# Kernel tuning notes

Measured on AMD Instinct MI355X. Metric: run time of the kernel, lower is better.

Reference implementation:

```python
import jax, jax.numpy as jnp
import numpy as np

SD = 4          # spixel_downsize
EPS = 1e-5      # BatchNorm eps
SLOPE = 0.01    # nn.LeakyReLU() default negative_slope


def deconv3d(x, w, stride, pad):
    # w is in torch ConvTranspose3d layout: (in_ch, out_ch, kd, kh, kw).
    # Transposed conv == conv with lhs_dilation=stride, flipped kernel,
    # padding (k-1-p) per spatial dim.
    kd, kh, kw = w.shape[2], w.shape[3], w.shape[4]
    wc = jnp.transpose(jnp.flip(w, axis=(2, 3, 4)), (1, 0, 2, 3, 4))  # OIDHW
    pads = [(kd - 1 - pad[0],) * 2, (kh - 1 - pad[1],) * 2, (kw - 1 - pad[2],) * 2]
    return jax.lax.conv_general_dilated(
        x, wc, window_strides=(1, 1, 1), padding=pads,
        lhs_dilation=(stride, stride, stride),
        dimension_numbers=('NCDHW', 'OIDHW', 'NCDHW'))


def bn_lrelu(x, g, b, relu=True):
    # inference BatchNorm3d with running_mean=0, running_var=1 (fresh BN)
    scale = (g / jnp.sqrt(1.0 + EPS)).reshape(1, -1, 1, 1, 1)
    y = x * scale + b.reshape(1, -1, 1, 1, 1)
    return jax.nn.leaky_relu(y, SLOPE) if relu else y


def _sl(s):
    # shift s in {+1, 0, -1} -> (agg slice, cost slice) along one spatial dim
    if s == 1:
        return slice(SD, None), slice(None, -SD)
    if s == 0:
        return slice(None), slice(None)
    return slice(None, -SD), slice(SD, None)


def setup_inputs() -> dict:
    key = jax.random.key(0)
    ks = jax.random.split(key, 8)
    b, d, h, w = 1, 24, 64, 128
    f32 = jnp.float32
    cv1 = jax.random.normal(ks[0], (b, 32, d, h, w), f32)                 # cv[-1]
    cv0 = jax.random.normal(ks[1], (b, 16, 2 * d, 2 * h, 2 * w), f32)     # cv[-2]
    sp = jax.random.uniform(ks[2], (b, 9, 4 * h, 4 * w), f32)             # superpixel probs
    w0a = jax.random.normal(ks[3], (32, 32, 3, 1, 1), f32) * 0.05
    w0b = jax.random.normal(ks[4], (32, 16, 4, 2, 2), f32) * 0.05
    w1a = jax.random.normal(ks[5], (32, 16, 3, 1, 1), f32) * 0.05
    w1b = jax.random.normal(ks[6], (16, 1, 4, 2, 2), f32) * 0.05
    g0, g1, g2, g3 = (jnp.ones((c,), f32) for c in (32, 16, 16, 1))
    b0, b1, b2, b3 = (jnp.zeros((c,), f32) for c in (32, 16, 16, 1))
    return dict(cv1=cv1, cv0=cv0, sp=sp, w0a=w0a, w0b=w0b, w1a=w1a, w1b=w1b,
                g0=g0, g1=g1, g2=g2, g3=g3, b0=b0, b1=b1, b2=b2, b3=b3)


def reference(cv1, cv0, sp, w0a, w0b, w1a, w1b, g0, g1, g2, g3, b0, b1, b2, b3):
    # conv[0]: BasicConv(32->32, k(3,1,1), s1, p(1,0,0)) + BasicConv(32->16, k(4,2,2), s2, p(1,0,0))
    x = bn_lrelu(deconv3d(cv1, w0a, 1, (1, 0, 0)), g0, b0)
    x = bn_lrelu(deconv3d(x, w0b, 2, (1, 0, 0)), g1, b1)
    x = jnp.concatenate((x, cv0), axis=1)
    # conv[1] (sp==2 branch): 32->16 then 16->out_dim, bn=relu=bnrelu=True
    x = bn_lrelu(deconv3d(x, w1a, 1, (1, 0, 0)), g2, b2)
    cost = bn_lrelu(deconv3d(x, w1b, 2, (1, 0, 0)), g3, b3)  # (b, 1, 4d, 4h, 4w)

    sp5 = sp[:, None]  # (b, 1, 9, H, W)
    agg = jnp.zeros_like(cost)
    k = 0
    for hy in (1, 0, -1):        # 9 fixed superpixel-neighbor shifts
        ah, ch = _sl(hy)
        for wx in (1, 0, -1):
            aw, cw = _sl(wx)
            wgt = sp5[:, :, k, ah, aw][:, :, None]  # (b,1,1,H',W')
            agg = agg.at[:, :, :, ah, aw].add(cost[:, :, :, ch, cw] * wgt)
            k += 1
    return agg
```

## Files before the change

kernel.cpp:

```cpp
#include <hip/hip_runtime.h>
#include <hip/hip_bf16.h>

typedef __hip_bfloat16 bf16;

constexpr int cD0 = 24,  cH0 = 64,  cW0 = 128;
constexpr int cD1 = 48,  cH1 = 128, cW1 = 256;
constexpr int cD2 = 96,  cH2 = 256, cW2 = 512;
constexpr size_t PL0 = (size_t)cD0 * cH0 * cW0;
constexpr size_t PL1 = (size_t)cD1 * cH1 * cW1;
constexpr size_t PL2 = (size_t)cD2 * cH2 * cW2;

__device__ __forceinline__ float b2f(bf16 v) { return __bfloat162float(v); }
__device__ __forceinline__ bf16  f2b(float v) { return __float2bfloat16(v); }
__device__ __forceinline__ float lrelu(float v) { return v >= 0.f ? v : 0.01f * v; }
__device__ __forceinline__ float us2f(ushort u) { return __uint_as_float(((uint)u) << 16); }
__device__ __forceinline__ ushort f2us(float v) { return __bfloat16_as_ushort(f2b(v)); }

__global__ __launch_bounds__(256) void kA(const float* __restrict__ cv1,
                                          const float* __restrict__ w0a,
                                          const float* __restrict__ g0,
                                          const float* __restrict__ b0,
                                          bf16* __restrict__ x1) {
    __shared__ float lw[3][32][32];
    __shared__ float lsc[32], lbi[32];
    const int tid = threadIdx.x;
    for (int i = tid; i < 32 * 32 * 3; i += 256) {
        int ci = i / 96, r = i - ci * 96, co = r / 3, u = r - co * 3;
        lw[u][ci][co] = w0a[i];
    }
    if (tid < 32) {
        lsc[tid] = g0[tid] * (1.0f / sqrtf(1.0f + 1e-5f));
        lbi[tid] = b0[tid];
    }
    __syncthreads();

    const int pos = blockIdx.x * 256 + tid;
    const int x = pos & (cW0 - 1);
    const int y = (pos >> 7) & (cH0 - 1);
    const int z = pos >> 13;

    float acc[32];
    #pragma unroll
    for (int co = 0; co < 32; ++co) acc[co] = 0.f;

    #pragma unroll
    for (int u = 0; u < 3; ++u) {
        const int zi = z + 1 - u;
        if (zi < 0 || zi >= cD0) continue;
        const float* src = cv1 + (size_t)(zi * cH0 + y) * cW0 + x;
        for (int ci = 0; ci < 32; ++ci) {
            const float v = src[ci * PL0];
            const float4* wp = (const float4*)&lw[u][ci][0];
            #pragma unroll
            for (int q = 0; q < 8; ++q) {
                float4 wv = wp[q];
                acc[4*q+0] += v * wv.x; acc[4*q+1] += v * wv.y;
                acc[4*q+2] += v * wv.z; acc[4*q+3] += v * wv.w;
            }
        }
    }
    #pragma unroll
    for (int co = 0; co < 32; ++co)
        x1[co * PL0 + (size_t)(z * cH0 + y) * cW0 + x] =
            f2b(lrelu(acc[co] * lsc[co] + lbi[co]));
}

__global__ __launch_bounds__(256) void kB(const bf16* __restrict__ x1,
                                          const float* __restrict__ w0b,
                                          const float* __restrict__ g1,
                                          const float* __restrict__ b1,
                                          bf16* __restrict__ x2) {
    __shared__ float lw[4][2][32][2][16];
    __shared__ float lsc[16], lbi[16];
    const int tid = threadIdx.x;
    for (int i = tid; i < 8192; i += 256) {
        int ci = i >> 8, co = (i >> 4) & 15, kd = (i >> 2) & 3, kh = (i >> 1) & 1, kw = i & 1;
        lw[kd][kh][ci][kw][co] = w0b[i];
    }
    if (tid < 16) {
        lsc[tid] = g1[tid] * (1.0f / sqrtf(1.0f + 1e-5f));
        lbi[tid] = b1[tid];
    }
    __syncthreads();

    const int t    = blockIdx.x * 256 + tid;
    const int lane = t & 63;
    const int row  = t >> 6;
    const int oh = row & 127, od = row >> 7;
    const int ih = oh >> 1, kh = oh & 1;
    const int p  = (od + 1) & 1;
    const int iw0 = 2 * lane;

    float acc[4][16];
    #pragma unroll
    for (int k = 0; k < 4; ++k)
        #pragma unroll
        for (int co = 0; co < 16; ++co) acc[k][co] = 0.f;

    #pragma unroll
    for (int j = 0; j < 2; ++j) {
        const int kd = p + 2 * j;
        const int id = (od + 1 - kd) >> 1;
        if (id < 0 || id >= cD0) continue;
        const bf16* src = x1 + (size_t)(id * cH0 + ih) * cW0 + iw0;
        #pragma unroll 4
        for (int ci = 0; ci < 32; ++ci) {
            const uint pk = *(const uint*)(src + ci * PL0);
            const float v0 = us2f((ushort)(pk & 0xffffu));
            const float v1 = us2f((ushort)(pk >> 16));
            const float4* wp0 = (const float4*)&lw[kd][kh][ci][0][0];
            const float4* wp1 = (const float4*)&lw[kd][kh][ci][1][0];
            #pragma unroll
            for (int q = 0; q < 4; ++q) {
                float4 w0 = wp0[q], w1 = wp1[q];
                acc[0][4*q+0] += v0 * w0.x; acc[0][4*q+1] += v0 * w0.y;
                acc[0][4*q+2] += v0 * w0.z; acc[0][4*q+3] += v0 * w0.w;
                acc[1][4*q+0] += v0 * w1.x; acc[1][4*q+1] += v0 * w1.y;
                acc[1][4*q+2] += v0 * w1.z; acc[1][4*q+3] += v0 * w1.w;
                acc[2][4*q+0] += v1 * w0.x; acc[2][4*q+1] += v1 * w0.y;
                acc[2][4*q+2] += v1 * w0.z; acc[2][4*q+3] += v1 * w0.w;
                acc[3][4*q+0] += v1 * w1.x; acc[3][4*q+1] += v1 * w1.y;
                acc[3][4*q+2] += v1 * w1.z; acc[3][4*q+3] += v1 * w1.w;
            }
        }
    }
    const size_t obase = (size_t)(od * cH1 + oh) * cW1 + 4 * lane;
    #pragma unroll
    for (int co = 0; co < 16; ++co) {
        ushort4 s;
        s.x = f2us(lrelu(acc[0][co] * lsc[co] + lbi[co]));
        s.y = f2us(lrelu(acc[1][co] * lsc[co] + lbi[co]));
        s.z = f2us(lrelu(acc[2][co] * lsc[co] + lbi[co]));
        s.w = f2us(lrelu(acc[3][co] * lsc[co] + lbi[co]));
        *(ushort4*)(x2 + co * PL1 + obase) = s;
    }
}

__global__ __launch_bounds__(256) void kD(const bf16* __restrict__ x2,
                                          const float* __restrict__ cv0,
                                          const float* __restrict__ w1a,
                                          const float* __restrict__ g2,
                                          const float* __restrict__ b2v,
                                          bf16* __restrict__ x3) {
    __shared__ float lw[3][32][16];
    __shared__ float lsc[16], lbi[16];
    const int tid = threadIdx.x;
    for (int i = tid; i < 1536; i += 256) {
        int ci = i / 48, r = i - ci * 48, co = r / 3, u = r - co * 3;
        lw[u][ci][co] = w1a[i];
    }
    if (tid < 16) {
        lsc[tid] = g2[tid] * (1.0f / sqrtf(1.0f + 1e-5f));
        lbi[tid] = b2v[tid];
    }
    __syncthreads();

    const int t    = blockIdx.x * 256 + tid;
    const int lane = t & 63;
    const int row  = t >> 6;
    const int y = row & 127, z = row >> 7;
    const int x0 = 4 * lane;

    float acc[4][16];
    #pragma unroll
    for (int k = 0; k < 4; ++k)
        #pragma unroll
        for (int co = 0; co < 16; ++co) acc[k][co] = 0.f;

    #pragma unroll
    for (int u = 0; u < 3; ++u) {
        const int zi = z + 1 - u;
        if (zi < 0 || zi >= cD1) continue;
        const size_t base = (size_t)(zi * cH1 + y) * cW1 + x0;
        #pragma unroll 4
        for (int ci = 0; ci < 16; ++ci) {
            const ushort4 pv = *(const ushort4*)(x2 + ci * PL1 + base);
            const float v0 = us2f(pv.x), v1 = us2f(pv.y);
            const float v2 = us2f(pv.z), v3 = us2f(pv.w);
            const float4* wp = (const float4*)&lw[u][ci][0];
            #pragma unroll
            for (int q = 0; q < 4; ++q) {
                float4 wv = wp[q];
                acc[0][4*q+0] += v0 * wv.x; acc[0][4*q+1] += v0 * wv.y;
                acc[0][4*q+2] += v0 * wv.z; acc[0][4*q+3] += v0 * wv.w;
                acc[1][4*q+0] += v1 * wv.x; acc[1][4*q+1] += v1 * wv.y;
                acc[1][4*q+2] += v1 * wv.z; acc[1][4*q+3] += v1 * wv.w;
                acc[2][4*q+0] += v2 * wv.x; acc[2][4*q+1] += v2 * wv.y;
                acc[2][4*q+2] += v2 * wv.z; acc[2][4*q+3] += v2 * wv.w;
                acc[3][4*q+0] += v3 * wv.x; acc[3][4*q+1] += v3 * wv.y;
                acc[3][4*q+2] += v3 * wv.z; acc[3][4*q+3] += v3 * wv.w;
            }
        }
        #pragma unroll 4
        for (int ci = 0; ci < 16; ++ci) {
            const float4 fv = *(const float4*)(cv0 + ci * PL1 + base);
            const float v0 = fv.x, v1 = fv.y, v2 = fv.z, v3 = fv.w;
            const float4* wp = (const float4*)&lw[u][16 + ci][0];
            #pragma unroll
            for (int q = 0; q < 4; ++q) {
                float4 wv = wp[q];
                acc[0][4*q+0] += v0 * wv.x; acc[0][4*q+1] += v0 * wv.y;
                acc[0][4*q+2] += v0 * wv.z; acc[0][4*q+3] += v0 * wv.w;
                acc[1][4*q+0] += v1 * wv.x; acc[1][4*q+1] += v1 * wv.y;
                acc[1][4*q+2] += v1 * wv.z; acc[1][4*q+3] += v1 * wv.w;
                acc[2][4*q+0] += v2 * wv.x; acc[2][4*q+1] += v2 * wv.y;
                acc[2][4*q+2] += v2 * wv.z; acc[2][4*q+3] += v2 * wv.w;
                acc[3][4*q+0] += v3 * wv.x; acc[3][4*q+1] += v3 * wv.y;
                acc[3][4*q+2] += v3 * wv.z; acc[3][4*q+3] += v3 * wv.w;
            }
        }
    }
    const size_t obase = (size_t)(z * cH1 + y) * cW1 + x0;
    #pragma unroll
    for (int co = 0; co < 16; ++co) {
        ushort4 s;
        s.x = f2us(lrelu(acc[0][co] * lsc[co] + lbi[co]));
        s.y = f2us(lrelu(acc[1][co] * lsc[co] + lbi[co]));
        s.z = f2us(lrelu(acc[2][co] * lsc[co] + lbi[co]));
        s.w = f2us(lrelu(acc[3][co] * lsc[co] + lbi[co]));
        *(ushort4*)(x3 + co * PL1 + obase) = s;
    }
}

__global__ __launch_bounds__(256) void kE(const bf16* __restrict__ x3,
                                          const float* __restrict__ w1b,
                                          const float* __restrict__ g3,
                                          const float* __restrict__ b3v,
                                          bf16* __restrict__ cost) {
    __shared__ float lw[256];
    const int tid = threadIdx.x;
    lw[tid] = w1b[tid];
    __syncthreads();

    const int t    = blockIdx.x * 256 + tid;
    const int lane = t & 63;
    const int rowq = t >> 6;
    const int iwp = lane + 64 * (rowq & 1);
    const int ih  = (rowq >> 1) & 127;
    const int od  = rowq >> 8;
    const int p   = (od + 1) & 1;
    const int iw0 = 2 * iwp;

    float a[2][2][2] = {};
    #pragma unroll
    for (int j = 0; j < 2; ++j) {
        const int kd = p + 2 * j;
        const int id = (od + 1 - kd) >> 1;
        if (id < 0 || id >= cD1) continue;
        const size_t base = (size_t)(id * cH1 + ih) * cW1 + iw0;
        #pragma unroll
        for (int ci = 0; ci < 16; ++ci) {
            const uint pk = *(const uint*)(x3 + ci * PL1 + base);
            const float v0 = us2f((ushort)(pk & 0xffffu));
            const float v1 = us2f((ushort)(pk >> 16));
            const float* w = &lw[ci * 16 + kd * 4];
            a[0][0][0] += v0 * w[0]; a[0][0][1] += v0 * w[1];
            a[0][1][0] += v0 * w[2]; a[0][1][1] += v0 * w[3];
            a[1][0][0] += v1 * w[0]; a[1][0][1] += v1 * w[1];
            a[1][1][0] += v1 * w[2]; a[1][1][1] += v1 * w[3];
        }
    }
    const float sc = g3[0] * (1.0f / sqrtf(1.0f + 1e-5f));
    const float bi = b3v[0];
    const size_t ob = (size_t)(od * cH2 + 2 * ih) * cW2 + 4 * iwp;
    ushort4 s;
    s.x = f2us(lrelu(a[0][0][0] * sc + bi));
    s.y = f2us(lrelu(a[0][0][1] * sc + bi));
    s.z = f2us(lrelu(a[1][0][0] * sc + bi));
    s.w = f2us(lrelu(a[1][0][1] * sc + bi));
    *(ushort4*)(cost + ob) = s;
    s.x = f2us(lrelu(a[0][1][0] * sc + bi));
    s.y = f2us(lrelu(a[0][1][1] * sc + bi));
    s.z = f2us(lrelu(a[1][1][0] * sc + bi));
    s.w = f2us(lrelu(a[1][1][1] * sc + bi));
    *(ushort4*)(cost + ob + cW2) = s;
}

__global__ __launch_bounds__(256) void kF(const bf16* __restrict__ cost,
                                          const float* __restrict__ sp,
                                          float* __restrict__ out) {
    const int t    = blockIdx.x * 256 + threadIdx.x;
    const int lane = t & 63;
    const int rowq = t >> 6;
    const int x0 = 4 * (lane + 64 * (rowq & 1));
    const int y  = (rowq >> 1) & 255;
    const int d0 = (rowq >> 9) * 4;
    const size_t plane = (size_t)cH2 * cW2;

    float4 wq[9];
    int cyc[3], cxc[3];
    #pragma unroll
    for (int r = 0; r < 3; ++r) {
        const int cy = y - 4 * (1 - r);
        const bool vy = (cy >= 0) && (cy < cH2);
        cyc[r] = vy ? cy : 0;
        #pragma unroll
        for (int c = 0; c < 3; ++c) {
            const int cx = x0 - 4 * (1 - c);
            const bool vx = (cx >= 0) && (cx < cW2);
            if (r == 0) cxc[c] = vx ? cx : 0;
            if (vy && vx)
                wq[r*3+c] = *(const float4*)(sp + (size_t)(r*3+c) * plane + (size_t)y * cW2 + x0);
            else
                wq[r*3+c] = make_float4(0.f, 0.f, 0.f, 0.f);
        }
    }
    #pragma unroll
    for (int dd = 0; dd < 4; ++dd) {
        const int d = d0 + dd;
        const bf16* cp = cost + (size_t)d * plane;
        float ax = 0.f, ay = 0.f, az = 0.f, aw = 0.f;
        #pragma unroll
        for (int r = 0; r < 3; ++r) {
            const bf16* rp = cp + (size_t)cyc[r] * cW2;
            #pragma unroll
            for (int c = 0; c < 3; ++c) {
                const ushort4 u = *(const ushort4*)(rp + cxc[c]);
                const float4 w = wq[r*3+c];
                ax += w.x * us2f(u.x); ay += w.y * us2f(u.y);
                az += w.z * us2f(u.z); aw += w.w * us2f(u.w);
            }
        }
        float4 o; o.x = ax; o.y = ay; o.z = az; o.w = aw;
        *(float4*)(out + (size_t)d * plane + (size_t)y * cW2 + x0) = o;
    }
}

extern "C" void kernel_launch(void* const* d_in, const int* in_sizes, int n_in,
                              void* d_out, int out_size, void* d_ws, size_t ws_size,
                              hipStream_t stream) {
    const float* cv1 = (const float*)d_in[0];
    const float* cv0 = (const float*)d_in[1];
    const float* sp  = (const float*)d_in[2];
    const float* w0a = (const float*)d_in[3];
    const float* w0b = (const float*)d_in[4];
    const float* w1a = (const float*)d_in[5];
    const float* w1b = (const float*)d_in[6];
    const float* g0  = (const float*)d_in[7];
    const float* g1  = (const float*)d_in[8];
    const float* g2  = (const float*)d_in[9];
    const float* g3  = (const float*)d_in[10];
    const float* b0  = (const float*)d_in[11];
    const float* b1  = (const float*)d_in[12];
    const float* b2  = (const float*)d_in[13];
    const float* b3  = (const float*)d_in[14];

    char* ws = (char*)d_ws;
    bf16* x1   = (bf16*)(ws);
    bf16* x2   = (bf16*)(ws + 12582912);
    bf16* x3   = (bf16*)(ws + 62914560);
    bf16* cost = (bf16*)(ws);

    kA<<<768,  256, 0, stream>>>(cv1, w0a, g0, b0, x1);
    kB<<<1536, 256, 0, stream>>>(x1, w0b, g1, b1, x2);
    kD<<<1536, 256, 0, stream>>>(x2, cv0, w1a, g2, b2, x3);
    kE<<<6144, 256, 0, stream>>>(x3, w1b, g3, b3, cost);
    kF<<<3072, 256, 0, stream>>>(cost, sp, (float*)d_out);
}
```

Baseline: 402.9 us.

## Remap wave-to-row assignment and interleave kw across lanes in deconv kernels

Kernels kC, kD and kE now give the four waves of a block four consecutive depth slices at the same (h) row instead of four consecutive h rows. Waves in a block therefore share overlapping input planes along depth, which may improve cache reuse. In kC each lane now handles a single kw parity and four input columns spaced 32 apart, so its bf16 stores are per-element and coalesced rather than ushort4. The trade-offs are scalar 2-byte loads and stores in place of packed accesses, and half the weights per lane in the inner loop.

Measured after the change: 383.5 us. 4.8% less time.

```diff
diff --git a/kernel.cpp b/kernel.cpp
--- a/kernel.cpp
+++ b/kernel.cpp
@@ -85,11 +85,14 @@
 
     const int t    = blockIdx.x * 256 + tid;
     const int lane = t & 63;
-    const int row  = t >> 6;
-    const int oh = row & 127, od = row >> 7;
+    const int wv_  = (t >> 6) & 3;
+    const int b_   = t >> 8;
+    const int oh = b_ & 127;
+    const int od = (b_ >> 7) * 4 + wv_;
     const int ih = oh >> 1, kh = oh & 1;
+    const int kw = lane & 1;
     const int p  = (od + 1) & 1;
-    const int iw0 = 2 * lane;
+    const int iwb = lane >> 1;
 
     float acc[4][16];
     #pragma unroll
@@ -102,38 +105,34 @@
         const int kd = p + 2 * j;
         const int id = (od + 1 - kd) >> 1;
         if (id < 0 || id >= cD0) continue;
-        const bf16* src = x1 + (size_t)(id * cH0 + ih) * cW0 + iw0;
-        #pragma unroll 4
+        const bf16* src = x1 + (size_t)(id * cH0 + ih) * cW0 + iwb;
         for (int ci = 0; ci < 32; ++ci) {
-            const uint pk = *(const uint*)(src + ci * PL0);
-            const float v0 = us2f((ushort)(pk & 0xffffu));
-            const float v1 = us2f((ushort)(pk >> 16));
-            const float4* wp0 = (const float4*)&lw[kd][kh][ci][0][0];
-            const float4* wp1 = (const float4*)&lw[kd][kh][ci][1][0];
+            const float v0 = b2f(src[ci * PL0 +  0]);
+            const float v1 = b2f(src[ci * PL0 + 32]);
+            const float v2 = b2f(src[ci * PL0 + 64]);
+            const float v3 = b2f(src[ci * PL0 + 96]);
+            const float4* wp = (const float4*)&lw[kd][kh][ci][kw][0];
             #pragma unroll
             for (int q = 0; q < 4; ++q) {
-                float4 w0 = wp0[q], w1 = wp1[q];
-                acc[0][4*q+0] += v0 * w0.x; acc[0][4*q+1] += v0 * w0.y;
-                acc[0][4*q+2] += v0 * w0.z; acc[0][4*q+3] += v0 * w0.w;
-                acc[1][4*q+0] += v0 * w1.x; acc[1][4*q+1] += v0 * w1.y;
-                acc[1][4*q+2] += v0 * w1.z; acc[1][4*q+3] += v0 * w1.w;
-                acc[2][4*q+0] += v1 * w0.x; acc[2][4*q+1] += v1 * w0.y;
-                acc[2][4*q+2] += v1 * w0.z; acc[2][4*q+3] += v1 * w0.w;
-                acc[3][4*q+0] += v1 * w1.x; acc[3][4*q+1] += v1 * w1.y;
-                acc[3][4*q+2] += v1 * w1.z; acc[3][4*q+3] += v1 * w1.w;
-            }
-        }
-    }
-    const size_t obase = (size_t)(od * cH1 + oh) * cW1 + 4 * lane;
-    #pragma unroll
-    for (int co = 0; co < 16; ++co) {
-        ushort4 s;
-        s.x = f2us(lrelu(acc[0][co] * lsc[co] + lbi[co]));
-        s.y = f2us(lrelu(acc[1][co] * lsc[co] + lbi[co]));
-        s.z = f2us(lrelu(acc[2][co] * lsc[co] + lbi[co]));
-        s.w = f2us(lrelu(acc[3][co] * lsc[co] + lbi[co]));
-        *(ushort4*)(x2 + co * PL1 + obase) = s;
-    }
+                float4 wv = wp[q];
+                acc[0][4*q+0] += v0 * wv.x; acc[0][4*q+1] += v0 * wv.y;
+                acc[0][4*q+2] += v0 * wv.z; acc[0][4*q+3] += v0 * wv.w;
+                acc[1][4*q+0] += v1 * wv.x; acc[1][4*q+1] += v1 * wv.y;
+                acc[1][4*q+2] += v1 * wv.z; acc[1][4*q+3] += v1 * wv.w;
+                acc[2][4*q+0] += v2 * wv.x; acc[2][4*q+1] += v2 * wv.y;
+                acc[2][4*q+2] += v2 * wv.z; acc[2][4*q+3] += v2 * wv.w;
+                acc[3][4*q+0] += v3 * wv.x; acc[3][4*q+1] += v3 * wv.y;
+                acc[3][4*q+2] += v3 * wv.z; acc[3][4*q+3] += v3 * wv.w;
+            }
+        }
+    }
+    const size_t obase = (size_t)(od * cH1 + oh) * cW1 + lane;
+    #pragma unroll
+    for (int k = 0; k < 4; ++k)
+        #pragma unroll
+        for (int co = 0; co < 16; ++co)
+            x2[co * PL1 + obase + 64 * k] =
+                f2b(lrelu(acc[k][co] * lsc[co] + lbi[co]));
 }
 
 __global__ __launch_bounds__(256) void kD(const bf16* __restrict__ x2,
@@ -157,8 +156,10 @@
 
     const int t    = blockIdx.x * 256 + tid;
     const int lane = t & 63;
-    const int row  = t >> 6;
-    const int y = row & 127, z = row >> 7;
+    const int wv_  = (t >> 6) & 3;
+    const int b_   = t >> 8;
+    const int y = b_ & 127;
+    const int z = (b_ >> 7) * 4 + wv_;
     const int x0 = 4 * lane;
 
     float acc[4][16];
@@ -234,10 +235,11 @@
 
     const int t    = blockIdx.x * 256 + tid;
     const int lane = t & 63;
-    const int rowq = t >> 6;
-    const int iwp = lane + 64 * (rowq & 1);
-    const int ih  = (rowq >> 1) & 127;
-    const int od  = rowq >> 8;
+    const int wv_  = (t >> 6) & 3;
+    const int b_   = t >> 8;
+    const int iwp = lane + 64 * (b_ & 1);
+    const int ih  = (b_ >> 1) & 127;
+    const int od  = (b_ >> 8) * 4 + wv_;
     const int p   = (od + 1) & 1;
     const int iw0 = 2 * iwp;
 
```
